# Performance work log

Measured on AMD Instinct MI355X. Metric: run time of the kernel, lower is better.

## Reference

```python
import jax, jax.numpy as jnp
import numpy as np

B, N, M = 512, 1024, 128
OUT_DIM, MOLVEC_DIM, IN_DIM = 256, 256, 512


def setup_inputs() -> dict:
    key = jax.random.key(0)
    ks = jax.random.split(key, 6)
    X = jax.random.normal(ks[0], (B, N, OUT_DIM), dtype=jnp.float32)
    molvec = jax.random.normal(ks[1], (B, MOLVEC_DIM), dtype=jnp.float32)
    idx_M = jax.random.randint(ks[2], (B, M), 0, N, dtype=jnp.int64)
    # Xavier-normal-ish scaled linear weights (torch layout: [out_features, in_features])
    fan_in1 = MOLVEC_DIM + OUT_DIM
    W1 = jax.random.normal(ks[3], (IN_DIM, fan_in1), dtype=jnp.float32) * jnp.sqrt(2.0 / (fan_in1 + IN_DIM))
    b1 = jnp.zeros((IN_DIM,), dtype=jnp.float32)
    W2 = jax.random.normal(ks[4], (IN_DIM, IN_DIM), dtype=jnp.float32) * jnp.sqrt(2.0 / (IN_DIM + IN_DIM))
    b2 = jnp.zeros((IN_DIM,), dtype=jnp.float32)
    return {"X": X, "molvec": molvec, "idx_M": idx_M, "W1": W1, "b1": b1, "W2": W2, "b2": b2}


def reference(X, molvec, idx_M, W1, b1, W2, b2):
    # Batched gather: replaces the per-sample index_select loop. [B, M, OUT_DIM]
    target_x = jnp.take_along_axis(X, idx_M[:, :, None], axis=1)
    # Broadcast molvec to each masked position and concat. [B, M, OUT_DIM+MOLVEC_DIM]
    mv = jnp.broadcast_to(molvec[:, None, :], (X.shape[0], idx_M.shape[1], molvec.shape[-1]))
    concat_x = jnp.concatenate([target_x, mv], axis=-1)
    # 2-layer MLP (fc1 -> relu -> fc2)
    h = jax.nn.relu(jnp.einsum('bmd,id->bmi', concat_x, W1) + b1)
    pred = jnp.einsum('bmi,oi->bmo', h, W2) + b2
    return pred.reshape(X.shape[0] * idx_M.shape[1], -1)
```

## Files before the change

kernel.cpp:

```cpp
#include <hip/hip_runtime.h>
#include <hip/hip_bf16.h>

#define BB 512
#define NN 1024
#define MM 128
#define OUTD 256
#define MOLD 256
#define IND 512
#define RROWS 65536

typedef float f32x4 __attribute__((ext_vector_type(4)));
typedef short s16x8 __attribute__((ext_vector_type(8)));
typedef __bf16 bf16x8 __attribute__((ext_vector_type(8)));

#define AS_GLOBAL const __attribute__((address_space(1))) void
#define AS_LDS __attribute__((address_space(3))) void

__device__ __forceinline__ unsigned short f2bf(float f) {
    unsigned int u = __builtin_bit_cast(unsigned int, f);
    u = (u + 0x7fffu + ((u >> 16) & 1u)) >> 16;
    return (unsigned short)u;
}

__global__ __launch_bounds__(256) void prep_weights(
    const float* __restrict__ W1, const float* __restrict__ W2,
    unsigned short* __restrict__ W1ab, unsigned short* __restrict__ W2b) {
    int i = blockIdx.x * 256 + threadIdx.x;
    float4 b = ((const float4*)W2)[i];
    ushort4 pb;
    pb.x = f2bf(b.x); pb.y = f2bf(b.y); pb.z = f2bf(b.z); pb.w = f2bf(b.w);
    ((ushort4*)W2b)[i] = pb;
    if (i < 32768) {
        int row = i >> 6, c4 = i & 63;
        float4 a = ((const float4*)(W1 + (size_t)row * 512))[c4];
        ushort4 pa;
        pa.x = f2bf(a.x); pa.y = f2bf(a.y); pa.z = f2bf(a.z); pa.w = f2bf(a.w);
        ((ushort4*)(W1ab + (size_t)row * 256))[c4] = pa;
    }
}

__global__ __launch_bounds__(256) void c1_kernel(
    const float* __restrict__ mol, const float* __restrict__ W1,
    const float* __restrict__ b1, float* __restrict__ C1) {
    __shared__ float ms[MOLD];
    const int b = blockIdx.x, t = threadIdx.x;
    ms[t] = mol[(size_t)b * MOLD + t];
    __syncthreads();
#pragma unroll
    for (int h = 0; h < 2; ++h) {
        const int n = h * 256 + t;
        const f32x4* w = (const f32x4*)(W1 + (size_t)n * 512 + 256);
        float acc = 0.f;
#pragma unroll 4
        for (int k4 = 0; k4 < 64; ++k4) {
            f32x4 wv = w[k4];
            acc += wv[0] * ms[k4 * 4 + 0];
            acc += wv[1] * ms[k4 * 4 + 1];
            acc += wv[2] * ms[k4 * 4 + 2];
            acc += wv[3] * ms[k4 * 4 + 3];
        }
        C1[(size_t)b * IND + n] = acc + b1[n];
    }
}

__global__ __launch_bounds__(256) void gather_kernel(
    const float* __restrict__ X, const int* __restrict__ idxp,
    unsigned short* __restrict__ Ag) {
    const int t = threadIdx.x;
    const int r = blockIdx.x * 8 + (t >> 5);
    const int l = t & 31;
    const int b = r >> 7;
    const int idx = idxp[r];
    const float* src = X + ((size_t)b * NN + idx) * OUTD + l * 8;
    float4 v0 = ((const float4*)src)[0];
    float4 v1 = ((const float4*)src)[1];
    ushort4 p0, p1;
    p0.x = f2bf(v0.x); p0.y = f2bf(v0.y); p0.z = f2bf(v0.z); p0.w = f2bf(v0.w);
    p1.x = f2bf(v1.x); p1.y = f2bf(v1.y); p1.z = f2bf(v1.z); p1.w = f2bf(v1.w);
    unsigned short* dst = Ag + (size_t)r * OUTD + l * 8;
    ((ushort4*)dst)[0] = p0;
    ((ushort4*)dst)[1] = p1;
}

__global__ __launch_bounds__(256) void gemm1_kernel(
    const unsigned short* __restrict__ Ag, const unsigned short* __restrict__ W1ab,
    const float* __restrict__ C1, unsigned short* __restrict__ H) {
    __shared__ __align__(16) unsigned short Asm[128 * 32];
    __shared__ __align__(16) unsigned short Bsm[128 * 32];

    const int t = threadIdx.x;
    const int lane = t & 63, w = t >> 6;
    const int b = blockIdx.x;
    const int row0 = b * 128;
    const int n0 = blockIdx.y * 128;
    const int wr = (w >> 1) * 64, wc = (w & 1) * 64;
    const int lr = lane & 15, quad = lane >> 4;

    f32x4 acc[4][4];
#pragma unroll
    for (int mi = 0; mi < 4; ++mi)
#pragma unroll
        for (int ni = 0; ni < 4; ++ni) acc[mi][ni] = {0.f, 0.f, 0.f, 0.f};

    for (int ki = 0; ki < 8; ++ki) {
        const int kt = ki * 32;
#pragma unroll
        for (int j = 0; j < 2; ++j) {
            const int cidx = j * 4 + w;
            const int s = cidx * 64 + lane;
            const unsigned short* ga = Ag + (size_t)(row0 + (s >> 2)) * OUTD + kt + (s & 3) * 8;
            __builtin_amdgcn_global_load_lds((AS_GLOBAL*)ga, (AS_LDS*)(Asm + cidx * 512), 16, 0, 0);
            const unsigned short* gb = W1ab + (size_t)(n0 + (s >> 2)) * OUTD + kt + (s & 3) * 8;
            __builtin_amdgcn_global_load_lds((AS_GLOBAL*)gb, (AS_LDS*)(Bsm + cidx * 512), 16, 0, 0);
        }
        __syncthreads();
        s16x8 af[4], bfr[4];
#pragma unroll
        for (int i = 0; i < 4; ++i)
            af[i] = *(const s16x8*)&Asm[(wr + i * 16 + lr) * 32 + quad * 8];
#pragma unroll
        for (int i = 0; i < 4; ++i)
            bfr[i] = *(const s16x8*)&Bsm[(wc + i * 16 + lr) * 32 + quad * 8];
#pragma unroll
        for (int mi = 0; mi < 4; ++mi)
#pragma unroll
            for (int ni = 0; ni < 4; ++ni)
                acc[mi][ni] = __builtin_amdgcn_mfma_f32_16x16x32_bf16(
                    __builtin_bit_cast(bf16x8, af[mi]),
                    __builtin_bit_cast(bf16x8, bfr[ni]), acc[mi][ni], 0, 0, 0);
        __syncthreads();
    }

    float bias[4];
#pragma unroll
    for (int ni = 0; ni < 4; ++ni) bias[ni] = C1[(size_t)b * IND + n0 + wc + ni * 16 + lr];
#pragma unroll
    for (int mi = 0; mi < 4; ++mi) {
#pragma unroll
        for (int ni = 0; ni < 4; ++ni) {
            const int gcol = n0 + wc + ni * 16 + lr;
#pragma unroll
            for (int rr = 0; rr < 4; ++rr) {
                const int grow = row0 + wr + mi * 16 + quad * 4 + rr;
                float v = acc[mi][ni][rr] + bias[ni];
                v = v > 0.f ? v : 0.f;
                H[(size_t)grow * IND + gcol] = f2bf(v);
            }
        }
    }
}

__global__ __launch_bounds__(256) void gemm2_kernel(
    const unsigned short* __restrict__ Hb, const unsigned short* __restrict__ W2b,
    const float* __restrict__ b2, float* __restrict__ out) {
    __shared__ __align__(16) unsigned short Asm[128 * 32];
    __shared__ __align__(16) unsigned short Bsm[128 * 32];

    const int t = threadIdx.x;
    const int lane = t & 63, w = t >> 6;
    const int row0 = blockIdx.x * 128;
    const int n0 = blockIdx.y * 128;
    const int wr = (w >> 1) * 64, wc = (w & 1) * 64;
    const int lr = lane & 15, quad = lane >> 4;

    f32x4 acc[4][4];
#pragma unroll
    for (int mi = 0; mi < 4; ++mi)
#pragma unroll
        for (int ni = 0; ni < 4; ++ni) acc[mi][ni] = {0.f, 0.f, 0.f, 0.f};

    for (int ki = 0; ki < 16; ++ki) {
        const int kt = ki * 32;
#pragma unroll
        for (int j = 0; j < 2; ++j) {
            const int cidx = j * 4 + w;
            const int s = cidx * 64 + lane;
            const unsigned short* ga = Hb + (size_t)(row0 + (s >> 2)) * IND + kt + (s & 3) * 8;
            __builtin_amdgcn_global_load_lds((AS_GLOBAL*)ga, (AS_LDS*)(Asm + cidx * 512), 16, 0, 0);
            const unsigned short* gb = W2b + (size_t)(n0 + (s >> 2)) * IND + kt + (s & 3) * 8;
            __builtin_amdgcn_global_load_lds((AS_GLOBAL*)gb, (AS_LDS*)(Bsm + cidx * 512), 16, 0, 0);
        }
        __syncthreads();
        s16x8 af[4], bfr[4];
#pragma unroll
        for (int i = 0; i < 4; ++i)
            af[i] = *(const s16x8*)&Asm[(wr + i * 16 + lr) * 32 + quad * 8];
#pragma unroll
        for (int i = 0; i < 4; ++i)
            bfr[i] = *(const s16x8*)&Bsm[(wc + i * 16 + lr) * 32 + quad * 8];
#pragma unroll
        for (int mi = 0; mi < 4; ++mi)
#pragma unroll
            for (int ni = 0; ni < 4; ++ni)
                acc[mi][ni] = __builtin_amdgcn_mfma_f32_16x16x32_bf16(
                    __builtin_bit_cast(bf16x8, af[mi]),
                    __builtin_bit_cast(bf16x8, bfr[ni]), acc[mi][ni], 0, 0, 0);
        __syncthreads();
    }

    float bias[4];
#pragma unroll
    for (int ni = 0; ni < 4; ++ni) bias[ni] = b2[n0 + wc + ni * 16 + lr];
#pragma unroll
    for (int mi = 0; mi < 4; ++mi) {
#pragma unroll
        for (int ni = 0; ni < 4; ++ni) {
            const int gcol = n0 + wc + ni * 16 + lr;
#pragma unroll
            for (int rr = 0; rr < 4; ++rr) {
                const int grow = row0 + wr + mi * 16 + quad * 4 + rr;
                out[(size_t)grow * IND + gcol] = acc[mi][ni][rr] + bias[ni];
            }
        }
    }
}

extern "C" void kernel_launch(void* const* d_in, const int* in_sizes, int n_in,
                              void* d_out, int out_size, void* d_ws, size_t ws_size,
                              hipStream_t stream) {
    const float* X = (const float*)d_in[0];
    const float* mol = (const float*)d_in[1];
    const int* idx = (const int*)d_in[2];
    const float* W1 = (const float*)d_in[3];
    const float* b1 = (const float*)d_in[4];
    const float* W2 = (const float*)d_in[5];
    const float* b2 = (const float*)d_in[6];
    float* out = (float*)d_out;

    unsigned short* W1ab = (unsigned short*)d_ws;
    unsigned short* W2b = W1ab + 512 * 256;
    float* C1 = (float*)(W2b + 512 * 512);
    unsigned short* Ag = (unsigned short*)(C1 + 512 * 512);
    unsigned short* H = Ag + (size_t)RROWS * OUTD;

    prep_weights<<<256, 256, 0, stream>>>(W1, W2, W1ab, W2b);
    c1_kernel<<<512, 256, 0, stream>>>(mol, W1, b1, C1);
    gather_kernel<<<8192, 256, 0, stream>>>(X, idx, Ag);
    gemm1_kernel<<<dim3(BB, IND / 128), 256, 0, stream>>>(Ag, W1ab, C1, H);
    gemm2_kernel<<<dim3(RROWS / 128, IND / 128), 256, 0, stream>>>(H, W2b, b2, out);
}
```

Measured before the change: 741.5 us.

## Fuse gather into GEMM1, keep gathered A tile resident in swizzled LDS

Result: no change. 728.0 us (-1.8%).

```diff
diff --git a/kernel.cpp b/kernel.cpp
--- a/kernel.cpp
+++ b/kernel.cpp
@@ -63,88 +63,94 @@
     }
 }
 
-__global__ __launch_bounds__(256) void gather_kernel(
+__global__ __launch_bounds__(256) void gemm1_fused(
     const float* __restrict__ X, const int* __restrict__ idxp,
-    unsigned short* __restrict__ Ag) {
-    const int t = threadIdx.x;
-    const int r = blockIdx.x * 8 + (t >> 5);
-    const int l = t & 31;
-    const int b = r >> 7;
-    const int idx = idxp[r];
-    const float* src = X + ((size_t)b * NN + idx) * OUTD + l * 8;
-    float4 v0 = ((const float4*)src)[0];
-    float4 v1 = ((const float4*)src)[1];
-    ushort4 p0, p1;
-    p0.x = f2bf(v0.x); p0.y = f2bf(v0.y); p0.z = f2bf(v0.z); p0.w = f2bf(v0.w);
-    p1.x = f2bf(v1.x); p1.y = f2bf(v1.y); p1.z = f2bf(v1.z); p1.w = f2bf(v1.w);
-    unsigned short* dst = Ag + (size_t)r * OUTD + l * 8;
-    ((ushort4*)dst)[0] = p0;
-    ((ushort4*)dst)[1] = p1;
-}
-
-__global__ __launch_bounds__(256) void gemm1_kernel(
-    const unsigned short* __restrict__ Ag, const unsigned short* __restrict__ W1ab,
-    const float* __restrict__ C1, unsigned short* __restrict__ H) {
-    __shared__ __align__(16) unsigned short Asm[128 * 32];
+    const unsigned short* __restrict__ W1ab, const float* __restrict__ C1,
+    unsigned short* __restrict__ H) {
+    __shared__ __align__(16) unsigned short A1[128 * 256];
     __shared__ __align__(16) unsigned short Bsm[128 * 32];
 
     const int t = threadIdx.x;
     const int lane = t & 63, w = t >> 6;
     const int b = blockIdx.x;
     const int row0 = b * 128;
-    const int n0 = blockIdx.y * 128;
     const int wr = (w >> 1) * 64, wc = (w & 1) * 64;
     const int lr = lane & 15, quad = lane >> 4;
 
-    f32x4 acc[4][4];
-#pragma unroll
-    for (int mi = 0; mi < 4; ++mi)
-#pragma unroll
-        for (int ni = 0; ni < 4; ++ni) acc[mi][ni] = {0.f, 0.f, 0.f, 0.f};
-
-    for (int ki = 0; ki < 8; ++ki) {
-        const int kt = ki * 32;
-#pragma unroll
-        for (int j = 0; j < 2; ++j) {
-            const int cidx = j * 4 + w;
-            const int s = cidx * 64 + lane;
-            const unsigned short* ga = Ag + (size_t)(row0 + (s >> 2)) * OUTD + kt + (s & 3) * 8;
-            __builtin_amdgcn_global_load_lds((AS_GLOBAL*)ga, (AS_LDS*)(Asm + cidx * 512), 16, 0, 0);
-            const unsigned short* gb = W1ab + (size_t)(n0 + (s >> 2)) * OUTD + kt + (s & 3) * 8;
-            __builtin_amdgcn_global_load_lds((AS_GLOBAL*)gb, (AS_LDS*)(Bsm + cidx * 512), 16, 0, 0);
-        }
-        __syncthreads();
-        s16x8 af[4], bfr[4];
-#pragma unroll
-        for (int i = 0; i < 4; ++i)
-            af[i] = *(const s16x8*)&Asm[(wr + i * 16 + lr) * 32 + quad * 8];
-#pragma unroll
-        for (int i = 0; i < 4; ++i)
-            bfr[i] = *(const s16x8*)&Bsm[(wc + i * 16 + lr) * 32 + quad * 8];
+#pragma unroll 4
+    for (int p = 0; p < 16; ++p) {
+        const int r = p * 8 + (t >> 5);
+        const int c = t & 31;
+        const int idxg = idxp[b * MM + r];
+        const float* src = X + ((size_t)b * NN + idxg) * OUTD + c * 8;
+        float4 v0 = ((const float4*)src)[0];
+        float4 v1 = ((const float4*)src)[1];
+        ushort4 p0, p1;
+        p0.x = f2bf(v0.x); p0.y = f2bf(v0.y); p0.z = f2bf(v0.z); p0.w = f2bf(v0.w);
+        p1.x = f2bf(v1.x); p1.y = f2bf(v1.y); p1.z = f2bf(v1.z); p1.w = f2bf(v1.w);
+        const int slot = c ^ (r & 7);
+        unsigned short* dst = &A1[r * 256 + slot * 8];
+        ((ushort4*)dst)[0] = p0;
+        ((ushort4*)dst)[1] = p1;
+    }
+    __syncthreads();
+
+    for (int nt = 0; nt < 4; ++nt) {
+        const int n0 = nt * 128;
+        f32x4 acc[4][4];
 #pragma unroll
         for (int mi = 0; mi < 4; ++mi)
 #pragma unroll
-            for (int ni = 0; ni < 4; ++ni)
-                acc[mi][ni] = __builtin_amdgcn_mfma_f32_16x16x32_bf16(
-                    __builtin_bit_cast(bf16x8, af[mi]),
-                    __builtin_bit_cast(bf16x8, bfr[ni]), acc[mi][ni], 0, 0, 0);
-        __syncthreads();
-    }
-
-    float bias[4];
-#pragma unroll
-    for (int ni = 0; ni < 4; ++ni) bias[ni] = C1[(size_t)b * IND + n0 + wc + ni * 16 + lr];
-#pragma unroll
-    for (int mi = 0; mi < 4; ++mi) {
-#pragma unroll
-        for (int ni = 0; ni < 4; ++ni) {
-            const int gcol = n0 + wc + ni * 16 + lr;
-#pragma unroll
-            for (int rr = 0; rr < 4; ++rr) {
-                const int grow = row0 + wr + mi * 16 + quad * 4 + rr;
-                float v = acc[mi][ni][rr] + bias[ni];
-                v = v > 0.f ? v : 0.f;
-                H[(size_t)grow * IND + gcol] = f2bf(v);
+            for (int ni = 0; ni < 4; ++ni) acc[mi][ni] = {0.f, 0.f, 0.f, 0.f};
+
+        for (int ki = 0; ki < 8; ++ki) {
+            const int kt = ki * 32;
+#pragma unroll
+            for (int j = 0; j < 2; ++j) {
+                const int cidx = j * 4 + w;
+                const int s = cidx * 64 + lane;
+                const unsigned short* gb =
+                    W1ab + (size_t)(n0 + (s >> 2)) * OUTD + kt + (s & 3) * 8;
+                __builtin_amdgcn_global_load_lds((AS_GLOBAL*)gb,
+                                                 (AS_LDS*)(Bsm + cidx * 512), 16, 0, 0);
+            }
+            __syncthreads();
+            s16x8 af[4], bfr[4];
+#pragma unroll
+            for (int i = 0; i < 4; ++i) {
+                const int ra = wr + i * 16 + lr;
+                const int sa = ((ki << 2) + quad) ^ (lr & 7);
+                af[i] = *(const s16x8*)&A1[ra * 256 + sa * 8];
+            }
+#pragma unroll
+            for (int i = 0; i < 4; ++i)
+                bfr[i] = *(const s16x8*)&Bsm[(wc + i * 16 + lr) * 32 + quad * 8];
+#pragma unroll
+            for (int mi = 0; mi < 4; ++mi)
+#pragma unroll
+                for (int ni = 0; ni < 4; ++ni)
+                    acc[mi][ni] = __builtin_amdgcn_mfma_f32_16x16x32_bf16(
+                        __builtin_bit_cast(bf16x8, af[mi]),
+                        __builtin_bit_cast(bf16x8, bfr[ni]), acc[mi][ni], 0, 0, 0);
+            __syncthreads();
+        }
+
+        float bias[4];
+#pragma unroll
+        for (int ni = 0; ni < 4; ++ni)
+            bias[ni] = C1[(size_t)b * IND + n0 + wc + ni * 16 + lr];
+#pragma unroll
+        for (int mi = 0; mi < 4; ++mi) {
+#pragma unroll
+            for (int ni = 0; ni < 4; ++ni) {
+                const int gcol = n0 + wc + ni * 16 + lr;
+#pragma unroll
+                for (int rr = 0; rr < 4; ++rr) {
+                    const int grow = row0 + wr + mi * 16 + quad * 4 + rr;
+                    float v = acc[mi][ni][rr] + bias[ni];
+                    v = v > 0.f ? v : 0.f;
+                    H[(size_t)grow * IND + gcol] = f2bf(v);
+                }
             }
         }
     }
@@ -230,12 +236,10 @@
     unsigned short* W1ab = (unsigned short*)d_ws;
     unsigned short* W2b = W1ab + 512 * 256;
     float* C1 = (float*)(W2b + 512 * 512);
-    unsigned short* Ag = (unsigned short*)(C1 + 512 * 512);
-    unsigned short* H = Ag + (size_t)RROWS * OUTD;
+    unsigned short* H = (unsigned short*)(C1 + 512 * 512);
 
     prep_weights<<<256, 256, 0, stream>>>(W1, W2, W1ab, W2b);
     c1_kernel<<<512, 256, 0, stream>>>(mol, W1, b1, C1);
-    gather_kernel<<<8192, 256, 0, stream>>>(X, idx, Ag);
-    gemm1_kernel<<<dim3(BB, IND / 128), 256, 0, stream>>>(Ag, W1ab, C1, H);
+    gemm1_fused<<<BB, 256, 0, stream>>>(X, idx, W1ab, C1, H);
     gemm2_kernel<<<dim3(RROWS / 128, IND / 128), 256, 0, stream>>>(H, W2b, b2, out);
 }
```
